# Kernel tuning notes

Hardware: AMD Instinct MI355X
Metric: run time of the kernel (lower is better)

The kernel has to match this reference:

```python
import jax, jax.numpy as jnp
import numpy as np

B, S, D_IN, D_OUT = 8, 2048, 1024, 1024


def setup_inputs() -> dict:
    key = jax.random.key(0)
    ks = jax.random.split(key, 9)
    sc = 1.0 / np.sqrt(D_IN)
    return {
        "in_k": jax.random.normal(ks[0], (B, S, D_IN), jnp.float32),
        "in_q": jax.random.normal(ks[1], (B, S, D_IN), jnp.float32),
        "in_v": jax.random.normal(ks[2], (B, S, D_IN), jnp.float32),
        "Wk": jax.random.normal(ks[3], (D_IN, D_OUT), jnp.float32) * sc,
        "bk": jax.random.normal(ks[4], (D_OUT,), jnp.float32) * sc,
        "Wq": jax.random.normal(ks[5], (D_IN, D_OUT), jnp.float32) * sc,
        "bq": jax.random.normal(ks[6], (D_OUT,), jnp.float32) * sc,
        "Wv": jax.random.normal(ks[7], (D_IN, D_OUT), jnp.float32) * sc,
        "bv": jax.random.normal(ks[8], (D_OUT,), jnp.float32) * sc,
    }


def reference(in_k, in_q, in_v, Wk, bk, Wq, bq, Wv, bv):
    k = in_k @ Wk + bk  # [B,S,D]
    q = in_q @ Wq + bq
    v = in_v @ Wv + bv
    scale = 1.0 / jnp.sqrt(jnp.asarray(D_OUT, q.dtype))
    scores = jnp.einsum("bqd,bkd->bqk", q, k) * scale  # [B,S,S]
    attn = jax.nn.softmax(scores, axis=-1)
    return jnp.einsum("bqk,bkd->bqd", attn, v)
```

## Files before the change

### kernel.cpp

```cpp
#include <hip/hip_runtime.h>
#include <hip/hip_bf16.h>
#include <stdint.h>

typedef __bf16 bf16x8 __attribute__((ext_vector_type(8)));
typedef float  f32x4  __attribute__((ext_vector_type(4)));

__device__ __forceinline__ uint16_t f32_to_bf16(float f) {
    union { float f; uint32_t u; } v; v.f = f;
    uint32_t u = v.u;
    uint32_t r = (u + 0x7FFFu + ((u >> 16) & 1u)) >> 16;
    return (uint16_t)r;
}

__device__ __forceinline__ void gld16(const void* g, void* l) {
    __builtin_amdgcn_global_load_lds(
        (const __attribute__((address_space(1))) void*)g,
        (__attribute__((address_space(3))) void*)l,
        16, 0, 0);
}

__global__ __launch_bounds__(256) void cast3_kernel(
    const float* __restrict__ i0, const float* __restrict__ i1,
    const float* __restrict__ i2, uint16_t* __restrict__ o0,
    uint16_t* __restrict__ o1, uint16_t* __restrict__ o2) {
    const float* in = (blockIdx.z == 0) ? i0 : (blockIdx.z == 1) ? i1 : i2;
    uint16_t* out = (blockIdx.z == 0) ? o0 : (blockIdx.z == 1) ? o1 : o2;
    size_t i = ((size_t)blockIdx.x * 256 + threadIdx.x) * 4;
    float4 f = *(const float4*)(in + i);
    ushort4 o;
    o.x = f32_to_bf16(f.x); o.y = f32_to_bf16(f.y);
    o.z = f32_to_bf16(f.z); o.w = f32_to_bf16(f.w);
    *(ushort4*)(out + i) = o;
}

__global__ __launch_bounds__(256) void wtrans_kernel(
    const float* __restrict__ W0, const float* __restrict__ W1,
    const float* __restrict__ W2, uint16_t* __restrict__ Wt0) {
    const float* W = (blockIdx.z == 0) ? W0 : (blockIdx.z == 1) ? W1 : W2;
    uint16_t* Wt = Wt0 + (size_t)blockIdx.z * 1024 * 1024;
    __shared__ float tile[64][65];
    const int n0 = blockIdx.x * 64, k0 = blockIdx.y * 64;
    const int tx = threadIdx.x & 63, ty0 = threadIdx.x >> 6;
#pragma unroll
    for (int r = 0; r < 16; ++r) {
        int ty = ty0 + r * 4;
        tile[ty][tx] = W[(size_t)(k0 + ty) * 1024 + n0 + tx];
    }
    __syncthreads();
#pragma unroll
    for (int r = 0; r < 16; ++r) {
        int ty = ty0 + r * 4;
        Wt[(size_t)(n0 + ty) * 1024 + k0 + tx] = f32_to_bf16(tile[tx][ty]);
    }
}

__global__ __launch_bounds__(256) void vtrans_kernel(
    const uint16_t* __restrict__ V, uint16_t* __restrict__ Vt) {
    const int b = blockIdx.z;
    const uint16_t* Vp = V + (size_t)b * 2048 * 1024;
    uint16_t* Vtp = Vt + (size_t)b * 1024 * 2048;
    __shared__ uint16_t tile[64][65];
    const int d0 = blockIdx.x * 64, s0 = blockIdx.y * 64;
    const int tx = threadIdx.x & 63, ty0 = threadIdx.x >> 6;
#pragma unroll
    for (int r = 0; r < 16; ++r) {
        int ty = ty0 + r * 4;
        tile[ty][tx] = Vp[(size_t)(s0 + ty) * 1024 + d0 + tx];
    }
    __syncthreads();
#pragma unroll
    for (int r = 0; r < 16; ++r) {
        int ty = ty0 + r * 4;
        Vtp[(size_t)(d0 + ty) * 2048 + s0 + tx] = tile[tx][ty];
    }
}

template <int EPI>
__global__ __launch_bounds__(256, 2) void gemm_nt_kernel(
    const uint16_t* __restrict__ A, long long lda, long long sAz,
    const uint16_t* __restrict__ B, long long ldb, long long sBz,
    void* __restrict__ Cv, long long ldc, long long sCz,
    int K, float alpha, const float* __restrict__ bias,
    float* __restrict__ sums, int Z, int tN) {
    __shared__ __align__(16) uint16_t As[128 * 32];
    __shared__ __align__(16) uint16_t Bs[128 * 32];

    const int tid  = threadIdx.x;
    const int lane = tid & 63;
    const int wave = tid >> 6;

    const int bid = blockIdx.x;
    const int z = bid % Z;
    const int t = bid / Z;
    const int bandSz = tN * 8;
    const int band = t / bandSz;
    const int r0 = t - band * bandSz;
    const int row0 = (band * 8 + (r0 & 7)) * 128;
    const int col0 = (r0 >> 3) * 128;

    A += (size_t)z * sAz;
    B += (size_t)z * sBz;

    const int c0 = tid, c1 = tid + 256;
    const int ar0 = c0 >> 2, ak0 = (((c0 & 3) ^ ((ar0 >> 1) & 3))) * 8;
    const int ar1 = c1 >> 2, ak1 = (((c1 & 3) ^ ((ar1 >> 1) & 3))) * 8;

    const int wr = wave >> 1, wc = wave & 1;
    const int mrow = lane & 15;
    const int quad = lane >> 4;
    const int qsw = (quad ^ ((mrow >> 1) & 3)) * 8;

    f32x4 acc[4][4];
#pragma unroll
    for (int i = 0; i < 4; ++i)
#pragma unroll
        for (int j = 0; j < 4; ++j) acc[i][j] = 0.0f;

    for (int k0 = 0; k0 < K; k0 += 32) {
        __syncthreads();
        gld16(A + (size_t)(row0 + ar0) * lda + k0 + ak0, &As[(size_t)c0 * 8]);
        gld16(A + (size_t)(row0 + ar1) * lda + k0 + ak1, &As[(size_t)c1 * 8]);
        gld16(B + (size_t)(col0 + ar0) * ldb + k0 + ak0, &Bs[(size_t)c0 * 8]);
        gld16(B + (size_t)(col0 + ar1) * ldb + k0 + ak1, &Bs[(size_t)c1 * 8]);
        __syncthreads();

        bf16x8 af[4], bfj[4];
#pragma unroll
        for (int i = 0; i < 4; ++i)
            af[i] = *(const bf16x8*)&As[(size_t)(wr * 64 + i * 16 + mrow) * 32 + qsw];
#pragma unroll
        for (int j = 0; j < 4; ++j)
            bfj[j] = *(const bf16x8*)&Bs[(size_t)(wc * 64 + j * 16 + mrow) * 32 + qsw];
#pragma unroll
        for (int i = 0; i < 4; ++i)
#pragma unroll
            for (int j = 0; j < 4; ++j)
                acc[i][j] = __builtin_amdgcn_mfma_f32_16x16x32_bf16(
                    af[i], bfj[j], acc[i][j], 0, 0, 0);
    }

    if (EPI == 0) {
        uint16_t* C = (uint16_t*)Cv + (size_t)z * sCz;
#pragma unroll
        for (int i = 0; i < 4; ++i)
#pragma unroll
            for (int j = 0; j < 4; ++j)
#pragma unroll
                for (int r = 0; r < 4; ++r) {
                    int row = row0 + wr * 64 + i * 16 + quad * 4 + r;
                    int col = col0 + wc * 64 + j * 16 + mrow;
                    C[(size_t)row * ldc + col] = f32_to_bf16(acc[i][j][r] + bias[col]);
                }
    } else if (EPI == 1) {
        uint16_t* C = (uint16_t*)Cv + (size_t)z * sCz;
        float rs[4][4];
#pragma unroll
        for (int i = 0; i < 4; ++i)
#pragma unroll
            for (int r = 0; r < 4; ++r) rs[i][r] = 0.0f;
#pragma unroll
        for (int i = 0; i < 4; ++i)
#pragma unroll
            for (int j = 0; j < 4; ++j)
#pragma unroll
                for (int r = 0; r < 4; ++r) {
                    int row = row0 + wr * 64 + i * 16 + quad * 4 + r;
                    int col = col0 + wc * 64 + j * 16 + mrow;
                    float e = __expf(acc[i][j][r] * alpha);
                    C[(size_t)row * ldc + col] = f32_to_bf16(e);
                    rs[i][r] += e;
                }
#pragma unroll
        for (int i = 0; i < 4; ++i)
#pragma unroll
            for (int r = 0; r < 4; ++r) {
                float s = rs[i][r];
                s += __shfl_xor(s, 1, 64);
                s += __shfl_xor(s, 2, 64);
                s += __shfl_xor(s, 4, 64);
                s += __shfl_xor(s, 8, 64);
                if (mrow == 0) {
                    int row = row0 + wr * 64 + i * 16 + quad * 4 + r;
                    atomicAdd(&sums[(size_t)z * 2048 + row], s);
                }
            }
    } else {
        float* C = (float*)Cv + (size_t)z * sCz;
        float inv[4][4];
#pragma unroll
        for (int i = 0; i < 4; ++i)
#pragma unroll
            for (int r = 0; r < 4; ++r) {
                int row = row0 + wr * 64 + i * 16 + quad * 4 + r;
                inv[i][r] = 1.0f / sums[(size_t)z * 2048 + row];
            }
#pragma unroll
        for (int i = 0; i < 4; ++i)
#pragma unroll
            for (int j = 0; j < 4; ++j)
#pragma unroll
                for (int r = 0; r < 4; ++r) {
                    int row = row0 + wr * 64 + i * 16 + quad * 4 + r;
                    int col = col0 + wc * 64 + j * 16 + mrow;
                    C[(size_t)row * ldc + col] = acc[i][j][r] * inv[i][r];
                }
    }
}

extern "C" void kernel_launch(void* const* d_in, const int* in_sizes, int n_in,
                              void* d_out, int out_size, void* d_ws, size_t ws_size,
                              hipStream_t stream) {
    const float* in_k = (const float*)d_in[0];
    const float* in_q = (const float*)d_in[1];
    const float* in_v = (const float*)d_in[2];
    const float* Wk = (const float*)d_in[3];
    const float* bk = (const float*)d_in[4];
    const float* Wq = (const float*)d_in[5];
    const float* bq = (const float*)d_in[6];
    const float* Wv = (const float*)d_in[7];
    const float* bv = (const float*)d_in[8];
    float* out = (float*)d_out;

    char* w = (char*)d_ws;
    uint16_t* Xq  = (uint16_t*)(w + 0);
    uint16_t* Xk  = (uint16_t*)(w + 33554432);
    uint16_t* Xv  = (uint16_t*)(w + 67108864);
    uint16_t* Qb  = (uint16_t*)(w + 100663296);
    uint16_t* Kb  = (uint16_t*)(w + 134217728);
    uint16_t* Vb  = (uint16_t*)(w + 167772160);
    uint16_t* Wqt = (uint16_t*)(w + 201326592);
    uint16_t* Wkt = Wqt + 1024 * 1024;
    uint16_t* Wvt = Wkt + 1024 * 1024;
    uint16_t* Sc  = Xq;
    uint16_t* Vt  = Xv;
    float*    sums = (float*)Vb;

    wtrans_kernel<<<dim3(16, 16, 3), 256, 0, stream>>>(Wq, Wk, Wv, Wqt);
    cast3_kernel<<<dim3(16384, 1, 3), 256, 0, stream>>>(in_q, in_k, in_v, Xq, Xk, Xv);

    gemm_nt_kernel<0><<<1024, 256, 0, stream>>>(
        Xq, 1024, 0, Wqt, 1024, 0, Qb, 1024, 0, 1024, 1.0f, bq, nullptr, 1, 8);
    gemm_nt_kernel<0><<<1024, 256, 0, stream>>>(
        Xk, 1024, 0, Wkt, 1024, 0, Kb, 1024, 0, 1024, 1.0f, bk, nullptr, 1, 8);
    gemm_nt_kernel<0><<<1024, 256, 0, stream>>>(
        Xv, 1024, 0, Wvt, 1024, 0, Vb, 1024, 0, 1024, 1.0f, bv, nullptr, 1, 8);

    vtrans_kernel<<<dim3(16, 32, 8), 256, 0, stream>>>(Vb, Vt);
    hipMemsetAsync(sums, 0, 8 * 2048 * sizeof(float), stream);

    gemm_nt_kernel<1><<<2048, 256, 0, stream>>>(
        Qb, 1024, 2048LL * 1024, Kb, 1024, 2048LL * 1024,
        Sc, 2048, 2048LL * 2048, 1024, 0.03125f, nullptr, sums, 8, 16);

    gemm_nt_kernel<2><<<1024, 256, 0, stream>>>(
        Sc, 2048, 2048LL * 2048, Vt, 2048, 1024LL * 2048,
        out, 1024, 2048LL * 1024, 2048, 1.0f, nullptr, sums, 8, 8);
}
```

Before: 534.8 us.

## Fuse three projection GEMMs into one launch and write V transposed directly

The three Q/K/V projection GEMMs are merged into a single 3072-block kernel that picks its input, weight and bias from the block index. The V projection writes its output transposed, so the separate transpose kernel and its extra pass over memory are gone. The cast kernel now handles 8 elements per thread, and the GEMM launch bounds rise to 4 blocks per CU. The transposed-V epilogue uses strided scattered 2-byte stores, and a higher occupancy target may cause register spills.

```diff
diff --git a/kernel.cpp b/kernel.cpp
--- a/kernel.cpp
+++ b/kernel.cpp
@@ -4,6 +4,7 @@
 
 typedef __bf16 bf16x8 __attribute__((ext_vector_type(8)));
 typedef float  f32x4  __attribute__((ext_vector_type(4)));
+typedef uint16_t u16x8 __attribute__((ext_vector_type(8)));
 
 __device__ __forceinline__ uint16_t f32_to_bf16(float f) {
     union { float f; uint32_t u; } v; v.f = f;
@@ -25,12 +26,15 @@
     uint16_t* __restrict__ o1, uint16_t* __restrict__ o2) {
     const float* in = (blockIdx.z == 0) ? i0 : (blockIdx.z == 1) ? i1 : i2;
     uint16_t* out = (blockIdx.z == 0) ? o0 : (blockIdx.z == 1) ? o1 : o2;
-    size_t i = ((size_t)blockIdx.x * 256 + threadIdx.x) * 4;
-    float4 f = *(const float4*)(in + i);
-    ushort4 o;
-    o.x = f32_to_bf16(f.x); o.y = f32_to_bf16(f.y);
-    o.z = f32_to_bf16(f.z); o.w = f32_to_bf16(f.w);
-    *(ushort4*)(out + i) = o;
+    size_t i = ((size_t)blockIdx.x * 256 + threadIdx.x) * 8;
+    float4 a = *(const float4*)(in + i);
+    float4 b = *(const float4*)(in + i + 4);
+    u16x8 o;
+    o[0] = f32_to_bf16(a.x); o[1] = f32_to_bf16(a.y);
+    o[2] = f32_to_bf16(a.z); o[3] = f32_to_bf16(a.w);
+    o[4] = f32_to_bf16(b.x); o[5] = f32_to_bf16(b.y);
+    o[6] = f32_to_bf16(b.z); o[7] = f32_to_bf16(b.w);
+    *(u16x8*)(out + i) = o;
 }
 
 __global__ __launch_bounds__(256) void wtrans_kernel(
@@ -54,34 +58,100 @@
     }
 }
 
-__global__ __launch_bounds__(256) void vtrans_kernel(
-    const uint16_t* __restrict__ V, uint16_t* __restrict__ Vt) {
-    const int b = blockIdx.z;
-    const uint16_t* Vp = V + (size_t)b * 2048 * 1024;
-    uint16_t* Vtp = Vt + (size_t)b * 1024 * 2048;
-    __shared__ uint16_t tile[64][65];
-    const int d0 = blockIdx.x * 64, s0 = blockIdx.y * 64;
-    const int tx = threadIdx.x & 63, ty0 = threadIdx.x >> 6;
-#pragma unroll
-    for (int r = 0; r < 16; ++r) {
-        int ty = ty0 + r * 4;
-        tile[ty][tx] = Vp[(size_t)(s0 + ty) * 1024 + d0 + tx];
-    }
-    __syncthreads();
-#pragma unroll
-    for (int r = 0; r < 16; ++r) {
-        int ty = ty0 + r * 4;
-        Vtp[(size_t)(d0 + ty) * 2048 + s0 + tx] = tile[tx][ty];
+__global__ __launch_bounds__(256, 4) void proj3_kernel(
+    const uint16_t* __restrict__ Ab, const uint16_t* __restrict__ Bb,
+    uint16_t* __restrict__ Cb, uint16_t* __restrict__ Vt,
+    const float* __restrict__ b0, const float* __restrict__ b1,
+    const float* __restrict__ b2) {
+    __shared__ __align__(16) uint16_t As[128 * 32];
+    __shared__ __align__(16) uint16_t Bs[128 * 32];
+
+    const int tid  = threadIdx.x;
+    const int lane = tid & 63;
+    const int wave = tid >> 6;
+
+    const int pidx = blockIdx.x >> 10;
+    const int t = blockIdx.x & 1023;
+    const int band = t >> 6;
+    const int r0 = t & 63;
+    const int row0 = (band * 8 + (r0 & 7)) * 128;
+    const int col0 = (r0 >> 3) * 128;
+
+    const uint16_t* A = Ab + (size_t)pidx * 16777216;
+    const uint16_t* B = Bb + (size_t)pidx * 1048576;
+    const float* bias = (pidx == 0) ? b0 : (pidx == 1) ? b1 : b2;
+
+    const int c0 = tid, c1 = tid + 256;
+    const int ar0 = c0 >> 2, ak0 = (((c0 & 3) ^ ((ar0 >> 1) & 3))) * 8;
+    const int ar1 = c1 >> 2, ak1 = (((c1 & 3) ^ ((ar1 >> 1) & 3))) * 8;
+
+    const int wr = wave >> 1, wc = wave & 1;
+    const int mrow = lane & 15;
+    const int quad = lane >> 4;
+    const int qsw = (quad ^ ((mrow >> 1) & 3)) * 8;
+
+    f32x4 acc[4][4];
+#pragma unroll
+    for (int i = 0; i < 4; ++i)
+#pragma unroll
+        for (int j = 0; j < 4; ++j) acc[i][j] = 0.0f;
+
+    for (int k0 = 0; k0 < 1024; k0 += 32) {
+        __syncthreads();
+        gld16(A + (size_t)(row0 + ar0) * 1024 + k0 + ak0, &As[(size_t)c0 * 8]);
+        gld16(A + (size_t)(row0 + ar1) * 1024 + k0 + ak1, &As[(size_t)c1 * 8]);
+        gld16(B + (size_t)(col0 + ar0) * 1024 + k0 + ak0, &Bs[(size_t)c0 * 8]);
+        gld16(B + (size_t)(col0 + ar1) * 1024 + k0 + ak1, &Bs[(size_t)c1 * 8]);
+        __syncthreads();
+
+        bf16x8 af[4], bfj[4];
+#pragma unroll
+        for (int i = 0; i < 4; ++i)
+            af[i] = *(const bf16x8*)&As[(size_t)(wr * 64 + i * 16 + mrow) * 32 + qsw];
+#pragma unroll
+        for (int j = 0; j < 4; ++j)
+            bfj[j] = *(const bf16x8*)&Bs[(size_t)(wc * 64 + j * 16 + mrow) * 32 + qsw];
+#pragma unroll
+        for (int i = 0; i < 4; ++i)
+#pragma unroll
+            for (int j = 0; j < 4; ++j)
+                acc[i][j] = __builtin_amdgcn_mfma_f32_16x16x32_bf16(
+                    af[i], bfj[j], acc[i][j], 0, 0, 0);
+    }
+
+    if (pidx < 2) {
+        uint16_t* C = Cb + (size_t)pidx * 16777216;
+#pragma unroll
+        for (int i = 0; i < 4; ++i)
+#pragma unroll
+            for (int j = 0; j < 4; ++j)
+#pragma unroll
+                for (int r = 0; r < 4; ++r) {
+                    int row = row0 + wr * 64 + i * 16 + quad * 4 + r;
+                    int col = col0 + wc * 64 + j * 16 + mrow;
+                    C[(size_t)row * 1024 + col] = f32_to_bf16(acc[i][j][r] + bias[col]);
+                }
+    } else {
+#pragma unroll
+        for (int i = 0; i < 4; ++i)
+#pragma unroll
+            for (int j = 0; j < 4; ++j)
+#pragma unroll
+                for (int r = 0; r < 4; ++r) {
+                    int row = row0 + wr * 64 + i * 16 + quad * 4 + r;
+                    int col = col0 + wc * 64 + j * 16 + mrow;
+                    Vt[((size_t)(row >> 11) * 1024 + col) * 2048 + (row & 2047)] =
+                        f32_to_bf16(acc[i][j][r] + bias[col]);
+                }
     }
 }
 
 template <int EPI>
-__global__ __launch_bounds__(256, 2) void gemm_nt_kernel(
+__global__ __launch_bounds__(256, 4) void gemm_nt_kernel(
     const uint16_t* __restrict__ A, long long lda, long long sAz,
     const uint16_t* __restrict__ B, long long ldb, long long sBz,
     void* __restrict__ Cv, long long ldc, long long sCz,
-    int K, float alpha, const float* __restrict__ bias,
-    float* __restrict__ sums, int Z, int tN) {
+    int K, float alpha, float* __restrict__ sums, int Z, int tN) {
     __shared__ __align__(16) uint16_t As[128 * 32];
     __shared__ __align__(16) uint16_t Bs[128 * 32];
 
@@ -139,19 +209,7 @@
                     af[i], bfj[j], acc[i][j], 0, 0, 0);
     }
 
-    if (EPI == 0) {
-        uint16_t* C = (uint16_t*)Cv + (size_t)z * sCz;
-#pragma unroll
-        for (int i = 0; i < 4; ++i)
-#pragma unroll
-            for (int j = 0; j < 4; ++j)
-#pragma unroll
-                for (int r = 0; r < 4; ++r) {
-                    int row = row0 + wr * 64 + i * 16 + quad * 4 + r;
-                    int col = col0 + wc * 64 + j * 16 + mrow;
-                    C[(size_t)row * ldc + col] = f32_to_bf16(acc[i][j][r] + bias[col]);
-                }
-    } else if (EPI == 1) {
+    if (EPI == 1) {
         uint16_t* C = (uint16_t*)Cv + (size_t)z * sCz;
         float rs[4][4];
 #pragma unroll
@@ -227,32 +285,23 @@
     uint16_t* Xv  = (uint16_t*)(w + 67108864);
     uint16_t* Qb  = (uint16_t*)(w + 100663296);
     uint16_t* Kb  = (uint16_t*)(w + 134217728);
-    uint16_t* Vb  = (uint16_t*)(w + 167772160);
+    uint16_t* Vt  = (uint16_t*)(w + 167772160);
     uint16_t* Wqt = (uint16_t*)(w + 201326592);
-    uint16_t* Wkt = Wqt + 1024 * 1024;
-    uint16_t* Wvt = Wkt + 1024 * 1024;
     uint16_t* Sc  = Xq;
-    uint16_t* Vt  = Xv;
-    float*    sums = (float*)Vb;
+    float*    sums = (float*)Xv;
 
     wtrans_kernel<<<dim3(16, 16, 3), 256, 0, stream>>>(Wq, Wk, Wv, Wqt);
-    cast3_kernel<<<dim3(16384, 1, 3), 256, 0, stream>>>(in_q, in_k, in_v, Xq, Xk, Xv);
-
-    gemm_nt_kernel<0><<<1024, 256, 0, stream>>>(
-        Xq, 1024, 0, Wqt, 1024, 0, Qb, 1024, 0, 1024, 1.0f, bq, nullptr, 1, 8);
-    gemm_nt_kernel<0><<<1024, 256, 0, stream>>>(
-        Xk, 1024, 0, Wkt, 1024, 0, Kb, 1024, 0, 1024, 1.0f, bk, nullptr, 1, 8);
-    gemm_nt_kernel<0><<<1024, 256, 0, stream>>>(
-        Xv, 1024, 0, Wvt, 1024, 0, Vb, 1024, 0, 1024, 1.0f, bv, nullptr, 1, 8);
-
-    vtrans_kernel<<<dim3(16, 32, 8), 256, 0, stream>>>(Vb, Vt);
+    cast3_kernel<<<dim3(8192, 1, 3), 256, 0, stream>>>(in_q, in_k, in_v, Xq, Xk, Xv);
+
+    proj3_kernel<<<3072, 256, 0, stream>>>(Xq, Wqt, Qb, Vt, bq, bk, bv);
+
     hipMemsetAsync(sums, 0, 8 * 2048 * sizeof(float), stream);
 
     gemm_nt_kernel<1><<<2048, 256, 0, stream>>>(
         Qb, 1024, 2048LL * 1024, Kb, 1024, 2048LL * 1024,
-        Sc, 2048, 2048LL * 2048, 1024, 0.03125f, nullptr, sums, 8, 16);
+        Sc, 2048, 2048LL * 2048, 1024, 0.03125f, sums, 8, 16);
 
     gemm_nt_kernel<2><<<1024, 256, 0, stream>>>(
         Sc, 2048, 2048LL * 2048, Vt, 2048, 1024LL * 2048,
-        out, 1024, 2048LL * 1024, 2048, 1.0f, nullptr, sums, 8, 8);
-}
+        out, 1024, 2048LL * 1024, 2048, 1.0f, sums, 8, 8);
+}
```

Result: no change. 526.8 us (-1.5%).
